# Kernel tuning notes

Measured on AMD Instinct MI355X. Metric: run time of the kernel, lower is better.

The kernel has to match this reference:

```python
import jax, jax.numpy as jnp
import numpy as np

C = 128       # in_channels
B = 256       # number of graph pairs (inter.shape[0])
N1_PER = 32   # nodes per graph, side 1
N2_PER = 32   # nodes per graph, side 2


def prelu(x, s):
    return jnp.where(x >= 0, x, s * x)


def _lin(k, fan_in, fan_out):
    return jax.random.normal(k, (fan_in, fan_out), jnp.float32) / np.sqrt(fan_in)


def setup_inputs() -> dict:
    key = jax.random.key(0)
    ks = jax.random.split(key, 16)
    N1, N2 = B * N1_PER, B * N2_PER
    d1 = np.full(B, N1_PER, np.int64)
    d2 = np.full(B, N2_PER, np.int64)
    batch_1 = np.repeat(np.arange(B), d1)
    batch_2 = np.repeat(np.arange(B), d2)
    # node offsets per graph (exclusive cumsum)
    s1 = np.concatenate([[0], np.cumsum(d1)[:-1]])
    s2 = np.concatenate([[0], np.cumsum(d2)[:-1]])
    # ragged pairwise cross-product indices, same as the torch loop
    ind_1 = np.concatenate([np.repeat(np.arange(d1[g]), d2[g]) + s1[g] for g in range(B)])
    ind_2 = np.concatenate([np.tile(np.arange(d2[g]), d1[g]) + s1[g] * 0 + s2[g] for g in range(B)])
    batch_ans = np.repeat(np.arange(B), d1 * d2)

    inp = {
        "x_1": jax.random.normal(ks[0], (N1, C), jnp.float32),
        "x_2": jax.random.normal(ks[1], (N2, C), jnp.float32),
        "inter": jax.random.normal(ks[2], (B, C), jnp.float32),
        "batch_1": jnp.asarray(batch_1, jnp.int32),
        "batch_2": jnp.asarray(batch_2, jnp.int32),
        "ind_1": jnp.asarray(ind_1, jnp.int32),
        "ind_2": jnp.asarray(ind_2, jnp.int32),
        "batch_ans": jnp.asarray(batch_ans, jnp.int32),
        # glorot-style param 'a'
        "a": jax.random.normal(ks[3], (C,), jnp.float32) * np.sqrt(2.0 / (1 + C)),
        # mlp: PReLU, Linear(2C,2C), PReLU, Linear(2C,C), PReLU, Linear(C,C)
        "Wm1": _lin(ks[4], 2 * C, 2 * C), "bm1": jnp.zeros((2 * C,), jnp.float32),
        "Wm2": _lin(ks[5], 2 * C, C),     "bm2": jnp.zeros((C,), jnp.float32),
        "Wm3": _lin(ks[6], C, C),         "bm3": jnp.zeros((C,), jnp.float32),
        "pm0": jnp.float32(0.25), "pm1": jnp.float32(0.25), "pm2": jnp.float32(0.25),
        # weight_1: Linear(2C,C), PReLU, Linear(C,1), Sigmoid
        "Wg1a": _lin(ks[7], 2 * C, C), "bg1a": jnp.zeros((C,), jnp.float32),
        "Wg1b": _lin(ks[8], C, 1),     "bg1b": jnp.zeros((1,), jnp.float32),
        "pw1": jnp.float32(0.25),
        # weight_2: Linear(2C,C), PReLU, Linear(C,1), Sigmoid
        "Wg2a": _lin(ks[9], 2 * C, C), "bg2a": jnp.zeros((C,), jnp.float32),
        "Wg2b": _lin(ks[10], C, 1),    "bg2b": jnp.zeros((1,), jnp.float32),
        "pw2": jnp.float32(0.25),
    }
    return inp


def reference(x_1, x_2, inter, batch_1, batch_2, ind_1, ind_2, batch_ans,
              a, Wm1, bm1, Wm2, bm2, Wm3, bm3, pm0, pm1, pm2,
              Wg1a, bg1a, Wg1b, bg1b, pw1, Wg2a, bg2a, Wg2b, bg2b, pw2):
    Bn = inter.shape[0]
    # global_add_pool readouts, broadcast back per node (repeat_interleave == gather by batch id)
    r1 = jax.ops.segment_sum(x_1, batch_1, num_segments=Bn)          # [B, C]
    r2 = jax.ops.segment_sum(x_2, batch_2, num_segments=Bn)          # [B, C]
    x1s = jnp.concatenate([x_1, r2[batch_1]], axis=1)                # [N1, 2C]
    x2s = jnp.concatenate([x_2, r1[batch_2]], axis=1)                # [N2, 2C]
    # gating MLPs -> sigmoid scalar per node
    w1 = jax.nn.sigmoid(prelu(x1s @ Wg1a + bg1a, pw1) @ Wg1b + bg1b)  # [N1, 1]
    w2 = jax.nn.sigmoid(prelu(x2s @ Wg2a + bg2a, pw2) @ Wg2b + bg2b)  # [N2, 1]
    x1g = x_1 * w1
    x2g = x_2 * w2
    # ragged pairwise gather
    xi = x1g[ind_1]                                                  # [P, C]
    xj = x2g[ind_2]                                                  # [P, C]
    h = jnp.concatenate([xi, xj], axis=1)                            # [P, 2C]
    h = prelu(h, pm0) @ Wm1 + bm1
    h = prelu(h, pm1) @ Wm2 + bm2
    h = prelu(h, pm2) @ Wm3 + bm3                                    # [P, C]
    ssi = (a * h) * inter[batch_ans]                                 # [P, C]
    logit = jax.ops.segment_sum(jnp.sum(ssi, axis=-1), batch_ans, num_segments=Bn)  # [B]
    return (logit, xi, xj)
```

## Files before the change

kernel.cpp:

```cpp
#include <hip/hip_runtime.h>
#include <hip/hip_bf16.h>
#include <hip/hip_fp16.h>

typedef __attribute__((ext_vector_type(8))) _Float16 half8;
typedef __attribute__((ext_vector_type(2))) _Float16 f16x2;
typedef __attribute__((ext_vector_type(8))) short short8;
typedef __attribute__((ext_vector_type(4))) float f32x4;

#define C_ 128

__device__ __forceinline__ unsigned short f2h(float f) {
    return __builtin_bit_cast(unsigned short, (_Float16)f);
}
__device__ __forceinline__ f16x2 pkrtz(float x, float y) {
    return __builtin_bit_cast(f16x2, __builtin_amdgcn_cvt_pkrtz(x, y));
}
__device__ __forceinline__ float prelu_f(float x, float s) {
    return fmaxf(x, 0.f) + s * fminf(x, 0.f);
}
__device__ __forceinline__ half8 prelu_h8(half8 x, half8 sl) {
    half8 z = {0, 0, 0, 0, 0, 0, 0, 0};
    half8 mx = __builtin_elementwise_max(x, z);
    half8 mn = __builtin_elementwise_min(x, z);
    return mn * sl + mx;
}

__global__ __launch_bounds__(256) void prep_weights(
    const float* __restrict__ Wm1, const float* __restrict__ Wm2,
    const float* __restrict__ Wg1a, const float* __restrict__ Wg2a,
    short* __restrict__ ws)
{
    int id = blockIdx.x * 256 + threadIdx.x;
    if (id < 8192) {
        int c = id >> 5, kb = (id & 31) * 8;
        short8 v;
        #pragma unroll
        for (int e = 0; e < 8; ++e) v[e] = (short)f2h(Wm1[(kb + e) * 256 + c]);
        *(short8*)(ws + c * 256 + kb) = v;
    }
    if (id < 4096) {
        int c = id >> 5, kb = (id & 31) * 8;
        short8 a, b, d;
        #pragma unroll
        for (int e = 0; e < 8; ++e) {
            a[e] = (short)f2h(Wm2 [(kb + e) * C_ + c]);
            b[e] = (short)f2h(Wg1a[(kb + e) * C_ + c]);
            d[e] = (short)f2h(Wg2a[(kb + e) * C_ + c]);
        }
        *(short8*)(ws + 65536  + c * 256 + kb) = a;
        *(short8*)(ws + 98304  + c * 256 + kb) = b;
        *(short8*)(ws + 131072 + c * 256 + kb) = d;
    }
}

__global__ __launch_bounds__(256) void reduce_out(
    const float* __restrict__ part, float* __restrict__ out)
{
    int t = threadIdx.x;
    out[t] = part[2 * t] + part[2 * t + 1];
}

__global__ __launch_bounds__(256, 2) void interactions_fused(
    const float* __restrict__ x1_, const float* __restrict__ x2_,
    const float* __restrict__ inter, const float* __restrict__ aP,
    const short* __restrict__ Wt,
    const float* __restrict__ bm1, const float* __restrict__ bm2,
    const float* __restrict__ Wm3, const float* __restrict__ bm3,
    const float* __restrict__ pm0p, const float* __restrict__ pm1p,
    const float* __restrict__ pm2p,
    const float* __restrict__ bg1a, const float* __restrict__ Wg1b,
    const float* __restrict__ bg1b, const float* __restrict__ pw1p,
    const float* __restrict__ bg2a, const float* __restrict__ Wg2b,
    const float* __restrict__ bg2b, const float* __restrict__ pw2p,
    float* __restrict__ part, float* __restrict__ out)
{
    __shared__ __align__(16) unsigned char regA[33792];
    __shared__ __align__(16) float rr[2][C_];
    __shared__ __align__(16) float tv[C_];
    __shared__ __align__(16) float ugs[C_];
    __shared__ float wgt[2][32];
    __shared__ float red[4];
    __shared__ float cbias_s;

    const int t = threadIdx.x;
    const int g = blockIdx.x >> 1;
    const int jh = blockIdx.x & 1;
    const int lane = t & 63;
    const int w = t >> 6;
    float* xs1 = (float*)regA;
    float* xs2 = (float*)(regA + 16896);

    {
        const float* s1 = x1_ + (size_t)g * 4096;
        const float* s2 = x2_ + (size_t)g * 4096;
        #pragma unroll
        for (int q = 0; q < 4; ++q) {
            int idx = q * 256 + t;
            int row = idx >> 5, cc = (idx & 31) * 4;
            float4 v1 = *(const float4*)(s1 + idx * 4);
            float4 v2 = *(const float4*)(s2 + idx * 4);
            *(float4*)(xs1 + row * 132 + cc) = v1;
            *(float4*)(xs2 + row * 132 + cc) = v2;
        }
    }
    __syncthreads();

    if (t < 128) {
        float s = 0.f;
        for (int n = 0; n < 32; ++n) s += xs1[n * 132 + t];
        rr[0][t] = s;
        tv[t] = aP[t] * inter[(size_t)g * C_ + t];
    } else {
        int c = t - 128;
        float s = 0.f;
        for (int n = 0; n < 32; ++n) s += xs2[n * 132 + c];
        rr[1][c] = s;
    }
    __syncthreads();

    if (t < 128) {
        const float* wr = Wm3 + t * C_;
        float s0 = 0, s1 = 0, s2 = 0, s3 = 0;
        #pragma unroll
        for (int k = 0; k < 128; k += 4) {
            float4 wv = *(const float4*)(wr + k);
            s0 += wv.x * tv[k];     s1 += wv.y * tv[k + 1];
            s2 += wv.z * tv[k + 2]; s3 += wv.w * tv[k + 3];
        }
        ugs[t] = (s0 + s1) + (s2 + s3);
    } else if (t < 192) {
        float p = bm3[lane] * tv[lane] + bm3[64 + lane] * tv[64 + lane];
        #pragma unroll
        for (int m = 1; m < 64; m <<= 1) p += __shfl_xor(p, m);
        if (lane == 0) cbias_s = p;
    }

    {
        const int sd = w >> 1;
        const int rt = w & 1;
        const float* xs = sd ? xs2 : xs1;
        const float* roth = sd ? rr[0] : rr[1];
        const short* WgT = Wt + (sd ? 131072 : 98304);
        const float* bga = sd ? bg2a : bg1a;
        const float* wgb = sd ? Wg2b : Wg1b;
        const float bgb = sd ? bg2b[0] : bg1b[0];
        const float pw  = sd ? pw2p[0] : pw1p[0];
        const int row = rt * 16 + (lane & 15);
        const int kg = (lane >> 4) * 8;

        half8 afr[8];
        #pragma unroll
        for (int kt = 0; kt < 8; ++kt) {
            const float* p = (kt < 4) ? (xs + row * 132 + kt * 32 + kg)
                                      : (roth + (kt - 4) * 32 + kg);
            float4 lo = *(const float4*)p;
            float4 hi = *(const float4*)(p + 4);
            f16x2 a = pkrtz(lo.x, lo.y);
            f16x2 b = pkrtz(lo.z, lo.w);
            f16x2 c = pkrtz(hi.x, hi.y);
            f16x2 d = pkrtz(hi.z, hi.w);
            half8 fr = {a[0], a[1], b[0], b[1], c[0], c[1], d[0], d[1]};
            afr[kt] = fr;
        }
        float pr[4] = {0, 0, 0, 0};
        #pragma unroll
        for (int ct = 0; ct < 8; ++ct) {
            const int c = ct * 16 + (lane & 15);
            const short* wp = WgT + c * 256 + kg;
            f32x4 acc = {0, 0, 0, 0};
            #pragma unroll
            for (int kt = 0; kt < 8; ++kt)
                acc = __builtin_amdgcn_mfma_f32_16x16x32_f16(
                          afr[kt], *(const half8*)(wp + kt * 32), acc, 0, 0, 0);
            const float bgac = bga[c], wgbc = wgb[c];
            #pragma unroll
            for (int r = 0; r < 4; ++r)
                pr[r] += prelu_f(acc[r] + bgac, pw) * wgbc;
        }
        #pragma unroll
        for (int r = 0; r < 4; ++r) {
            float p = pr[r];
            p += __shfl_xor(p, 1); p += __shfl_xor(p, 2);
            p += __shfl_xor(p, 4); p += __shfl_xor(p, 8);
            if ((lane & 15) == 0)
                wgt[sd][rt * 16 + (lane >> 4) * 4 + r] =
                    1.f / (1.f + __expf(-(p + bgb)));
        }
    }
    __syncthreads();

    float4 sl1[4], sl2[4];
    {
        const int cc = (t & 31) * 4;
        const int tn = t >> 5;
        #pragma unroll
        for (int m = 0; m < 4; ++m) {
            const int nr = m * 8 + tn;
            const float w1v = wgt[0][nr], w2v = wgt[1][nr];
            float4 v1 = *(float4*)(xs1 + nr * 132 + cc);
            float4 v2 = *(float4*)(xs2 + nr * 132 + cc);
            v1.x *= w1v; v1.y *= w1v; v1.z *= w1v; v1.w *= w1v;
            v2.x *= w2v; v2.y *= w2v; v2.z *= w2v; v2.w *= w2v;
            *(float4*)(xs1 + nr * 132 + cc) = v1;
            *(float4*)(xs2 + nr * 132 + cc) = v2;
            sl1[m] = v1; sl2[m] = v2;
        }
    }
    __syncthreads();

    {
        const int sd = w >> 1;
        const int rt = w & 1;
        const float* xs = sd ? xs2 : xs1;
        const float pm0 = pm0p[0];
        const int row = rt * 16 + (lane & 15);
        const int kg = (lane >> 4) * 8;
        half8 afr[4];
        #pragma unroll
        for (int kt = 0; kt < 4; ++kt) {
            const float* p = xs + row * 132 + kt * 32 + kg;
            float4 lo = *(const float4*)p;
            float4 hi = *(const float4*)(p + 4);
            f16x2 a = pkrtz(prelu_f(lo.x, pm0), prelu_f(lo.y, pm0));
            f16x2 b = pkrtz(prelu_f(lo.z, pm0), prelu_f(lo.w, pm0));
            f16x2 c = pkrtz(prelu_f(hi.x, pm0), prelu_f(hi.y, pm0));
            f16x2 d = pkrtz(prelu_f(hi.z, pm0), prelu_f(hi.w, pm0));
            half8 fr = {a[0], a[1], b[0], b[1], c[0], c[1], d[0], d[1]};
            afr[kt] = fr;
        }
        f32x4 acc[16];
        #pragma unroll
        for (int ct = 0; ct < 16; ++ct) {
            const int c = ct * 16 + (lane & 15);
            const short* wp = Wt + c * 256 + sd * 128 + kg;
            f32x4 av = {0, 0, 0, 0};
            #pragma unroll
            for (int kt = 0; kt < 4; ++kt)
                av = __builtin_amdgcn_mfma_f32_16x16x32_f16(
                         afr[kt], *(const half8*)(wp + kt * 32), av, 0, 0, 0);
            acc[ct] = av;
        }
        __syncthreads();
        unsigned char* dst = regA + (sd ? 16896 : 0);
        #pragma unroll
        for (int ct = 0; ct < 16; ++ct) {
            const int c = ct * 16 + (lane & 15);
            const float badd = sd ? 0.f : bm1[c];
            #pragma unroll
            for (int r = 0; r < 4; ++r) {
                const int n = rt * 16 + (lane >> 4) * 4 + r;
                const int off = n * 512 + ((2 * c + ((n & 7) << 6)) & 511);
                *(unsigned short*)(dst + off) = f2h(acc[ct][r] + badd);
            }
        }
    }
    __syncthreads();

    {
        const float pm1v = pm1p[0], pm2v = pm2p[0];
        const _Float16 pm1s = (_Float16)pm1v;
        const half8 pm1h = {pm1s, pm1s, pm1s, pm1s, pm1s, pm1s, pm1s, pm1s};
        const int cl = lane & 15;
        const int kg8 = (lane >> 4) * 8;
        const int kg16 = kg8 * 2;
        const int c0 = (2 * w) * 16 + cl, c1 = (2 * w + 1) * 16 + cl;
        half8 Bf0[8], Bf1[8];
        const short* w2p0 = Wt + 65536 + c0 * 256 + kg8;
        const short* w2p1 = Wt + 65536 + c1 * 256 + kg8;
        #pragma unroll
        for (int kt = 0; kt < 8; ++kt) {
            Bf0[kt] = *(const half8*)(w2p0 + kt * 32);
            Bf1[kt] = *(const half8*)(w2p1 + kt * 32);
        }
        const float bm2c0 = bm2[c0], bm2c1 = bm2[c1];
        const float ug0 = ugs[c0], ug1 = ugs[c1];
        const unsigned char* Ub = regA;
        const unsigned char* Vb = regA + 16896;

        half8 Vr[8];
        {
            const int j0 = jh * 16 + cl;
            const int vs = (j0 & 7) << 6;
            #pragma unroll
            for (int kt = 0; kt < 8; ++kt) {
                const int koff = kt * 64 + kg16;
                Vr[kt] = *(const half8*)(Vb + j0 * 512 + ((koff + vs) & 511));
            }
        }

        float* oxi = out + 256 + (size_t)g * 131072;
        float* oxj = out + 256 + 33554432 + (size_t)g * 131072;
        const int cc = (t & 31) * 4;
        const int tn = t >> 5;
        float psum = 0.f;

        #pragma unroll
        for (int rh = 0; rh < 2; ++rh) {
            const int n0 = rh * 16 + tn;
            const int n1 = rh * 16 + 8 + tn;
            const float4 s1a = sl1[rh * 2], s1b = sl1[rh * 2 + 1];
            const float4 s2a = sl2[rh * 2], s2b = sl2[rh * 2 + 1];
            #pragma unroll 2
            for (int ii = 0; ii < 16; ++ii) {
                const int i = rh * 16 + ii;
                const int ub = i * 512, us = (i & 7) << 6;
                half8 u8[8];
                #pragma unroll
                for (int kt = 0; kt < 8; ++kt)
                    u8[kt] = *(const half8*)(Ub + ub + ((kt * 64 + kg16 + us) & 511));
                f32x4 acc0 = {0, 0, 0, 0}, acc1 = {0, 0, 0, 0};
                #pragma unroll
                for (int kt = 0; kt < 8; ++kt) {
                    half8 af = prelu_h8(u8[kt] + Vr[kt], pm1h);
                    acc0 = __builtin_amdgcn_mfma_f32_16x16x32_f16(af, Bf0[kt], acc0, 0, 0, 0);
                    acc1 = __builtin_amdgcn_mfma_f32_16x16x32_f16(af, Bf1[kt], acc1, 0, 0, 0);
                }
                #pragma unroll
                for (int r = 0; r < 4; ++r) {
                    psum += prelu_f(acc0[r] + bm2c0, pm2v) * ug0;
                    psum += prelu_f(acc1[r] + bm2c1, pm2v) * ug1;
                }
                const int jj = jh * 16 + ii;
                *(float4*)(oxi + (size_t)(n0 * 32 + jj) * 128 + cc) = s1a;
                *(float4*)(oxi + (size_t)(n1 * 32 + jj) * 128 + cc) = s1b;
                *(float4*)(oxj + (size_t)(jj * 32 + n0) * 128 + cc) = s2a;
                *(float4*)(oxj + (size_t)(jj * 32 + n1) * 128 + cc) = s2b;
            }
        }
        #pragma unroll
        for (int m = 1; m < 64; m <<= 1) psum += __shfl_xor(psum, m);
        if (lane == 0) red[w] = psum;
    }
    __syncthreads();
    if (t == 0)
        part[blockIdx.x] = red[0] + red[1] + red[2] + red[3] + 512.f * cbias_s;
}

extern "C" void kernel_launch(void* const* d_in, const int* in_sizes, int n_in,
                              void* d_out, int out_size, void* d_ws, size_t ws_size,
                              hipStream_t stream) {
    const float* x1   = (const float*)d_in[0];
    const float* x2   = (const float*)d_in[1];
    const float* itr  = (const float*)d_in[2];
    const float* a    = (const float*)d_in[8];
    const float* Wm1  = (const float*)d_in[9];
    const float* bm1  = (const float*)d_in[10];
    const float* Wm2  = (const float*)d_in[11];
    const float* bm2  = (const float*)d_in[12];
    const float* Wm3  = (const float*)d_in[13];
    const float* bm3  = (const float*)d_in[14];
    const float* pm0  = (const float*)d_in[15];
    const float* pm1  = (const float*)d_in[16];
    const float* pm2  = (const float*)d_in[17];
    const float* Wg1a = (const float*)d_in[18];
    const float* bg1a = (const float*)d_in[19];
    const float* Wg1b = (const float*)d_in[20];
    const float* bg1b = (const float*)d_in[21];
    const float* pw1  = (const float*)d_in[22];
    const float* Wg2a = (const float*)d_in[23];
    const float* bg2a = (const float*)d_in[24];
    const float* Wg2b = (const float*)d_in[25];
    const float* bg2b = (const float*)d_in[26];
    const float* pw2  = (const float*)d_in[27];
    float* out = (float*)d_out;
    short* Wt = (short*)d_ws;
    float* part = (float*)(Wt + 163840);

    hipLaunchKernelGGL(prep_weights, dim3(32), dim3(256), 0, stream,
                       Wm1, Wm2, Wg1a, Wg2a, Wt);
    hipLaunchKernelGGL(interactions_fused, dim3(512), dim3(256), 0, stream,
                       x1, x2, itr, a, Wt, bm1, bm2, Wm3, bm3,
                       pm0, pm1, pm2, bg1a, Wg1b, bg1b, pw1,
                       bg2a, Wg2b, bg2b, pw2, part, out);
    hipLaunchKernelGGL(reduce_out, dim3(1), dim3(256), 0, stream,
                       part, out);
}
```

Baseline: 92.86 us.

## Warp-specialize one block per graph: MFMA waves compute while store waves write xi/xj

Each graph now runs as one 512-thread block instead of two 256-thread blocks. Four waves do the gating, the first layer and the pairwise MLP over all 32x32 pairs. The other four waves compute the Wm3 projection and stream the replicated xi/xj outputs with nontemporal stores, and the two groups coordinate through LDS atomic counters instead of full barriers. The final logit is written straight from the block, so the separate reduce kernel and its launch are gone. The intent is to overlap the large output writes with MFMA work and avoid duplicating the first layer across two blocks. The cost is lower occupancy (one block per CU) and spin-waiting on shared counters.

```diff
diff --git a/kernel.cpp b/kernel.cpp
--- a/kernel.cpp
+++ b/kernel.cpp
@@ -53,14 +53,7 @@
     }
 }
 
-__global__ __launch_bounds__(256) void reduce_out(
-    const float* __restrict__ part, float* __restrict__ out)
-{
-    int t = threadIdx.x;
-    out[t] = part[2 * t] + part[2 * t + 1];
-}
-
-__global__ __launch_bounds__(256, 2) void interactions_fused(
+__global__ __launch_bounds__(512, 1) void interactions_fused(
     const float* __restrict__ x1_, const float* __restrict__ x2_,
     const float* __restrict__ inter, const float* __restrict__ aP,
     const short* __restrict__ Wt,
@@ -72,35 +65,38 @@
     const float* __restrict__ bg1b, const float* __restrict__ pw1p,
     const float* __restrict__ bg2a, const float* __restrict__ Wg2b,
     const float* __restrict__ bg2b, const float* __restrict__ pw2p,
-    float* __restrict__ part, float* __restrict__ out)
+    float* __restrict__ out)
 {
-    __shared__ __align__(16) unsigned char regA[33792];
+    __shared__ __align__(16) float xs1[32 * 132];
+    __shared__ __align__(16) float xs2[32 * 132];
+    __shared__ __align__(16) unsigned char Ub[16384];
+    __shared__ __align__(16) unsigned char Vb[16384];
     __shared__ __align__(16) float rr[2][C_];
     __shared__ __align__(16) float tv[C_];
     __shared__ __align__(16) float ugs[C_];
-    __shared__ float wgt[2][32];
+    __shared__ float wgtp[2][2][32];
     __shared__ float red[4];
     __shared__ float cbias_s;
+    __shared__ int cnt1, cnt2;
 
     const int t = threadIdx.x;
-    const int g = blockIdx.x >> 1;
-    const int jh = blockIdx.x & 1;
+    const int g = blockIdx.x;
     const int lane = t & 63;
     const int w = t >> 6;
-    float* xs1 = (float*)regA;
-    float* xs2 = (float*)(regA + 16896);
+
+    if (t == 0) { cnt1 = 0; cnt2 = 0; }
 
     {
         const float* s1 = x1_ + (size_t)g * 4096;
         const float* s2 = x2_ + (size_t)g * 4096;
         #pragma unroll
-        for (int q = 0; q < 4; ++q) {
-            int idx = q * 256 + t;
+        for (int q = 0; q < 2; ++q) {
+            int idx = q * 512 + t;
             int row = idx >> 5, cc = (idx & 31) * 4;
-            float4 v1 = *(const float4*)(s1 + idx * 4);
-            float4 v2 = *(const float4*)(s2 + idx * 4);
-            *(float4*)(xs1 + row * 132 + cc) = v1;
-            *(float4*)(xs2 + row * 132 + cc) = v2;
+            f32x4 v1 = *(const f32x4*)(s1 + idx * 4);
+            f32x4 v2 = *(const f32x4*)(s2 + idx * 4);
+            *(f32x4*)(xs1 + row * 132 + cc) = v1;
+            *(f32x4*)(xs2 + row * 132 + cc) = v2;
         }
     }
     __syncthreads();
@@ -109,41 +105,27 @@
         float s = 0.f;
         for (int n = 0; n < 32; ++n) s += xs1[n * 132 + t];
         rr[0][t] = s;
-        tv[t] = aP[t] * inter[(size_t)g * C_ + t];
-    } else {
+    } else if (t < 256) {
         int c = t - 128;
         float s = 0.f;
         for (int n = 0; n < 32; ++n) s += xs2[n * 132 + c];
         rr[1][c] = s;
+    } else if (t < 384) {
+        int c = t - 256;
+        tv[c] = aP[c] * inter[(size_t)g * C_ + c];
     }
     __syncthreads();
 
-    if (t < 128) {
-        const float* wr = Wm3 + t * C_;
-        float s0 = 0, s1 = 0, s2 = 0, s3 = 0;
-        #pragma unroll
-        for (int k = 0; k < 128; k += 4) {
-            float4 wv = *(const float4*)(wr + k);
-            s0 += wv.x * tv[k];     s1 += wv.y * tv[k + 1];
-            s2 += wv.z * tv[k + 2]; s3 += wv.w * tv[k + 3];
-        }
-        ugs[t] = (s0 + s1) + (s2 + s3);
-    } else if (t < 192) {
-        float p = bm3[lane] * tv[lane] + bm3[64 + lane] * tv[64 + lane];
-        #pragma unroll
-        for (int m = 1; m < 64; m <<= 1) p += __shfl_xor(p, m);
-        if (lane == 0) cbias_s = p;
-    }
-
     {
-        const int sd = w >> 1;
-        const int rt = w & 1;
+        const int task = w & 3;
+        const int half = w >> 2;
+        const int sd = task >> 1;
+        const int rt = task & 1;
         const float* xs = sd ? xs2 : xs1;
         const float* roth = sd ? rr[0] : rr[1];
         const short* WgT = Wt + (sd ? 131072 : 98304);
         const float* bga = sd ? bg2a : bg1a;
         const float* wgb = sd ? Wg2b : Wg1b;
-        const float bgb = sd ? bg2b[0] : bg1b[0];
         const float pw  = sd ? pw2p[0] : pw1p[0];
         const int row = rt * 16 + (lane & 15);
         const int kg = (lane >> 4) * 8;
@@ -153,18 +135,19 @@
         for (int kt = 0; kt < 8; ++kt) {
             const float* p = (kt < 4) ? (xs + row * 132 + kt * 32 + kg)
                                       : (roth + (kt - 4) * 32 + kg);
-            float4 lo = *(const float4*)p;
-            float4 hi = *(const float4*)(p + 4);
-            f16x2 a = pkrtz(lo.x, lo.y);
-            f16x2 b = pkrtz(lo.z, lo.w);
-            f16x2 c = pkrtz(hi.x, hi.y);
-            f16x2 d = pkrtz(hi.z, hi.w);
+            f32x4 lo = *(const f32x4*)p;
+            f32x4 hi = *(const f32x4*)(p + 4);
+            f16x2 a = pkrtz(lo[0], lo[1]);
+            f16x2 b = pkrtz(lo[2], lo[3]);
+            f16x2 c = pkrtz(hi[0], hi[1]);
+            f16x2 d = pkrtz(hi[2], hi[3]);
             half8 fr = {a[0], a[1], b[0], b[1], c[0], c[1], d[0], d[1]};
             afr[kt] = fr;
         }
         float pr[4] = {0, 0, 0, 0};
         #pragma unroll
-        for (int ct = 0; ct < 8; ++ct) {
+        for (int cq = 0; cq < 4; ++cq) {
+            const int ct = half * 4 + cq;
             const int c = ct * 16 + (lane & 15);
             const short* wp = WgT + c * 256 + kg;
             f32x4 acc = {0, 0, 0, 0};
@@ -183,157 +166,197 @@
             p += __shfl_xor(p, 1); p += __shfl_xor(p, 2);
             p += __shfl_xor(p, 4); p += __shfl_xor(p, 8);
             if ((lane & 15) == 0)
-                wgt[sd][rt * 16 + (lane >> 4) * 4 + r] =
-                    1.f / (1.f + __expf(-(p + bgb)));
+                wgtp[half][sd][rt * 16 + (lane >> 4) * 4 + r] = p;
         }
     }
     __syncthreads();
 
-    float4 sl1[4], sl2[4];
     {
+        const float bgb1 = bg1b[0], bgb2 = bg2b[0];
         const int cc = (t & 31) * 4;
         const int tn = t >> 5;
         #pragma unroll
-        for (int m = 0; m < 4; ++m) {
-            const int nr = m * 8 + tn;
-            const float w1v = wgt[0][nr], w2v = wgt[1][nr];
-            float4 v1 = *(float4*)(xs1 + nr * 132 + cc);
-            float4 v2 = *(float4*)(xs2 + nr * 132 + cc);
-            v1.x *= w1v; v1.y *= w1v; v1.z *= w1v; v1.w *= w1v;
-            v2.x *= w2v; v2.y *= w2v; v2.z *= w2v; v2.w *= w2v;
-            *(float4*)(xs1 + nr * 132 + cc) = v1;
-            *(float4*)(xs2 + nr * 132 + cc) = v2;
-            sl1[m] = v1; sl2[m] = v2;
+        for (int m = 0; m < 2; ++m) {
+            const int nr = m * 16 + tn;
+            const float w1v = 1.f / (1.f + __expf(-(wgtp[0][0][nr] + wgtp[1][0][nr] + bgb1)));
+            const float w2v = 1.f / (1.f + __expf(-(wgtp[0][1][nr] + wgtp[1][1][nr] + bgb2)));
+            f32x4 v1 = *(f32x4*)(xs1 + nr * 132 + cc);
+            f32x4 v2 = *(f32x4*)(xs2 + nr * 132 + cc);
+            v1 *= w1v; v2 *= w2v;
+            *(f32x4*)(xs1 + nr * 132 + cc) = v1;
+            *(f32x4*)(xs2 + nr * 132 + cc) = v2;
         }
     }
     __syncthreads();
 
-    {
-        const int sd = w >> 1;
-        const int rt = w & 1;
-        const float* xs = sd ? xs2 : xs1;
-        const float pm0 = pm0p[0];
-        const int row = rt * 16 + (lane & 15);
-        const int kg = (lane >> 4) * 8;
-        half8 afr[4];
-        #pragma unroll
-        for (int kt = 0; kt < 4; ++kt) {
-            const float* p = xs + row * 132 + kt * 32 + kg;
-            float4 lo = *(const float4*)p;
-            float4 hi = *(const float4*)(p + 4);
-            f16x2 a = pkrtz(prelu_f(lo.x, pm0), prelu_f(lo.y, pm0));
-            f16x2 b = pkrtz(prelu_f(lo.z, pm0), prelu_f(lo.w, pm0));
-            f16x2 c = pkrtz(prelu_f(hi.x, pm0), prelu_f(hi.y, pm0));
-            f16x2 d = pkrtz(prelu_f(hi.z, pm0), prelu_f(hi.w, pm0));
-            half8 fr = {a[0], a[1], b[0], b[1], c[0], c[1], d[0], d[1]};
-            afr[kt] = fr;
-        }
-        f32x4 acc[16];
-        #pragma unroll
-        for (int ct = 0; ct < 16; ++ct) {
-            const int c = ct * 16 + (lane & 15);
-            const short* wp = Wt + c * 256 + sd * 128 + kg;
-            f32x4 av = {0, 0, 0, 0};
-            #pragma unroll
-            for (int kt = 0; kt < 4; ++kt)
-                av = __builtin_amdgcn_mfma_f32_16x16x32_f16(
-                         afr[kt], *(const half8*)(wp + kt * 32), av, 0, 0, 0);
-            acc[ct] = av;
-        }
-        __syncthreads();
-        unsigned char* dst = regA + (sd ? 16896 : 0);
-        #pragma unroll
-        for (int ct = 0; ct < 16; ++ct) {
-            const int c = ct * 16 + (lane & 15);
-            const float badd = sd ? 0.f : bm1[c];
-            #pragma unroll
-            for (int r = 0; r < 4; ++r) {
-                const int n = rt * 16 + (lane >> 4) * 4 + r;
-                const int off = n * 512 + ((2 * c + ((n & 7) << 6)) & 511);
-                *(unsigned short*)(dst + off) = f2h(acc[ct][r] + badd);
-            }
-        }
-    }
-    __syncthreads();
-
-    {
-        const float pm1v = pm1p[0], pm2v = pm2p[0];
-        const _Float16 pm1s = (_Float16)pm1v;
-        const half8 pm1h = {pm1s, pm1s, pm1s, pm1s, pm1s, pm1s, pm1s, pm1s};
-        const int cl = lane & 15;
-        const int kg8 = (lane >> 4) * 8;
-        const int kg16 = kg8 * 2;
-        const int c0 = (2 * w) * 16 + cl, c1 = (2 * w + 1) * 16 + cl;
-        half8 Bf0[8], Bf1[8];
-        const short* w2p0 = Wt + 65536 + c0 * 256 + kg8;
-        const short* w2p1 = Wt + 65536 + c1 * 256 + kg8;
-        #pragma unroll
-        for (int kt = 0; kt < 8; ++kt) {
-            Bf0[kt] = *(const half8*)(w2p0 + kt * 32);
-            Bf1[kt] = *(const half8*)(w2p1 + kt * 32);
-        }
-        const float bm2c0 = bm2[c0], bm2c1 = bm2[c1];
-        const float ug0 = ugs[c0], ug1 = ugs[c1];
-        const unsigned char* Ub = regA;
-        const unsigned char* Vb = regA + 16896;
-
-        half8 Vr[8];
-        {
-            const int j0 = jh * 16 + cl;
-            const int vs = (j0 & 7) << 6;
-            #pragma unroll
-            for (int kt = 0; kt < 8; ++kt) {
-                const int koff = kt * 64 + kg16;
-                Vr[kt] = *(const half8*)(Vb + j0 * 512 + ((koff + vs) & 511));
-            }
-        }
-
+    if (w >= 4) {
+        if (t < 384) {
+            const int c = t - 256;
+            const float* wr = Wm3 + c * C_;
+            float s0 = 0, s1 = 0, s2 = 0, s3 = 0;
+            #pragma unroll
+            for (int k = 0; k < 128; k += 4) {
+                f32x4 wv = *(const f32x4*)(wr + k);
+                s0 += wv[0] * tv[k];     s1 += wv[1] * tv[k + 1];
+                s2 += wv[2] * tv[k + 2]; s3 += wv[3] * tv[k + 3];
+            }
+            ugs[c] = (s0 + s1) + (s2 + s3);
+        } else if (w == 7) {
+            float p = bm3[lane] * tv[lane] + bm3[64 + lane] * tv[64 + lane];
+            #pragma unroll
+            for (int m = 1; m < 64; m <<= 1) p += __shfl_xor(p, m);
+            if (lane == 0) cbias_s = p;
+        }
+        __threadfence_block();
+        if (lane == 0)
+            __hip_atomic_fetch_add(&cnt1, 1, __ATOMIC_RELEASE, __HIP_MEMORY_SCOPE_WORKGROUP);
+
+        const int ws_ = w - 4;
         float* oxi = out + 256 + (size_t)g * 131072;
         float* oxj = out + 256 + 33554432 + (size_t)g * 131072;
-        const int cc = (t & 31) * 4;
-        const int tn = t >> 5;
+        const int ccl = (lane & 31) * 4;
+
+        #pragma unroll
+        for (int blk = 0; blk < 8; ++blk) {
+            const int i = ws_ * 8 + blk;
+            f32x4 v = *(const f32x4*)(xs1 + i * 132 + ccl);
+            float* base = oxi + i * 4096 + lane * 4;
+            #pragma unroll
+            for (int s2 = 0; s2 < 16; ++s2)
+                __builtin_nontemporal_store(v, (f32x4*)(base + s2 * 256));
+        }
+        f32x4 vj[16];
+        #pragma unroll
+        for (int s2 = 0; s2 < 16; ++s2) {
+            const int jn = (2 * s2 + (lane >> 5)) & 31;
+            vj[s2] = *(const f32x4*)(xs2 + jn * 132 + ccl);
+        }
+        #pragma unroll
+        for (int so = 0; so < 8; ++so) {
+            float* bb = oxj + (size_t)(ws_ * 256 + so * 32) * 128 + lane * 4;
+            #pragma unroll
+            for (int s2 = 0; s2 < 16; ++s2)
+                __builtin_nontemporal_store(vj[s2], (f32x4*)(bb + s2 * 256));
+        }
+    } else {
+        {
+            const int sd = w >> 1;
+            const int rt = w & 1;
+            const float* xs = sd ? xs2 : xs1;
+            const float pm0 = pm0p[0];
+            const int row = rt * 16 + (lane & 15);
+            const int kg = (lane >> 4) * 8;
+            half8 afr[4];
+            #pragma unroll
+            for (int kt = 0; kt < 4; ++kt) {
+                const float* p = xs + row * 132 + kt * 32 + kg;
+                f32x4 lo = *(const f32x4*)p;
+                f32x4 hi = *(const f32x4*)(p + 4);
+                f16x2 a = pkrtz(prelu_f(lo[0], pm0), prelu_f(lo[1], pm0));
+                f16x2 b = pkrtz(prelu_f(lo[2], pm0), prelu_f(lo[3], pm0));
+                f16x2 c = pkrtz(prelu_f(hi[0], pm0), prelu_f(hi[1], pm0));
+                f16x2 d = pkrtz(prelu_f(hi[2], pm0), prelu_f(hi[3], pm0));
+                half8 fr = {a[0], a[1], b[0], b[1], c[0], c[1], d[0], d[1]};
+                afr[kt] = fr;
+            }
+            unsigned char* dst = sd ? Vb : Ub;
+            #pragma unroll
+            for (int ct = 0; ct < 16; ++ct) {
+                const int c = ct * 16 + (lane & 15);
+                const short* wp = Wt + c * 256 + sd * 128 + kg;
+                f32x4 av = {0, 0, 0, 0};
+                #pragma unroll
+                for (int kt = 0; kt < 4; ++kt)
+                    av = __builtin_amdgcn_mfma_f32_16x16x32_f16(
+                             afr[kt], *(const half8*)(wp + kt * 32), av, 0, 0, 0);
+                const float badd = sd ? 0.f : bm1[c];
+                #pragma unroll
+                for (int r = 0; r < 4; ++r) {
+                    const int n = rt * 16 + (lane >> 4) * 4 + r;
+                    const int off = n * 512 + ((2 * c + ((n & 7) << 6)) & 511);
+                    *(unsigned short*)(dst + off) = f2h(av[r] + badd);
+                }
+            }
+        }
+        __threadfence_block();
+        if (lane == 0)
+            __hip_atomic_fetch_add(&cnt1, 1, __ATOMIC_RELEASE, __HIP_MEMORY_SCOPE_WORKGROUP);
+        while (__hip_atomic_load(&cnt1, __ATOMIC_ACQUIRE, __HIP_MEMORY_SCOPE_WORKGROUP) < 8)
+            __builtin_amdgcn_s_sleep(1);
+        __threadfence_block();
+
         float psum = 0.f;
-
-        #pragma unroll
-        for (int rh = 0; rh < 2; ++rh) {
-            const int n0 = rh * 16 + tn;
-            const int n1 = rh * 16 + 8 + tn;
-            const float4 s1a = sl1[rh * 2], s1b = sl1[rh * 2 + 1];
-            const float4 s2a = sl2[rh * 2], s2b = sl2[rh * 2 + 1];
+        {
+            const float pm1v = pm1p[0], pm2v = pm2p[0];
+            const _Float16 pm1s = (_Float16)pm1v;
+            const half8 pm1h = {pm1s, pm1s, pm1s, pm1s, pm1s, pm1s, pm1s, pm1s};
+            const int cl = lane & 15;
+            const int kg8 = (lane >> 4) * 8;
+            const int kg16 = kg8 * 2;
+            const int c0 = (2 * w) * 16 + cl, c1 = (2 * w + 1) * 16 + cl;
+            half8 Bf0[8], Bf1[8];
+            const short* w2p0 = Wt + 65536 + c0 * 256 + kg8;
+            const short* w2p1 = Wt + 65536 + c1 * 256 + kg8;
+            #pragma unroll
+            for (int kt = 0; kt < 8; ++kt) {
+                Bf0[kt] = *(const half8*)(w2p0 + kt * 32);
+                Bf1[kt] = *(const half8*)(w2p1 + kt * 32);
+            }
+            const float bm2c0 = bm2[c0], bm2c1 = bm2[c1];
+            const float ug0 = ugs[c0], ug1 = ugs[c1];
+
+            half8 VrA[8], VrB[8];
+            {
+                const int j0 = cl, j1 = 16 + cl;
+                #pragma unroll
+                for (int kt = 0; kt < 8; ++kt) {
+                    const int koff = kt * 64 + kg16;
+                    VrA[kt] = *(const half8*)(Vb + j0 * 512 + ((koff + ((j0 & 7) << 6)) & 511));
+                    VrB[kt] = *(const half8*)(Vb + j1 * 512 + ((koff + ((j1 & 7) << 6)) & 511));
+                }
+            }
+
             #pragma unroll 2
-            for (int ii = 0; ii < 16; ++ii) {
-                const int i = rh * 16 + ii;
+            for (int i = 0; i < 32; ++i) {
                 const int ub = i * 512, us = (i & 7) << 6;
                 half8 u8[8];
                 #pragma unroll
                 for (int kt = 0; kt < 8; ++kt)
                     u8[kt] = *(const half8*)(Ub + ub + ((kt * 64 + kg16 + us) & 511));
                 f32x4 acc0 = {0, 0, 0, 0}, acc1 = {0, 0, 0, 0};
+                f32x4 acc2 = {0, 0, 0, 0}, acc3 = {0, 0, 0, 0};
                 #pragma unroll
                 for (int kt = 0; kt < 8; ++kt) {
-                    half8 af = prelu_h8(u8[kt] + Vr[kt], pm1h);
-                    acc0 = __builtin_amdgcn_mfma_f32_16x16x32_f16(af, Bf0[kt], acc0, 0, 0, 0);
-                    acc1 = __builtin_amdgcn_mfma_f32_16x16x32_f16(af, Bf1[kt], acc1, 0, 0, 0);
+                    half8 afA = prelu_h8(u8[kt] + VrA[kt], pm1h);
+                    half8 afB = prelu_h8(u8[kt] + VrB[kt], pm1h);
+                    acc0 = __builtin_amdgcn_mfma_f32_16x16x32_f16(afA, Bf0[kt], acc0, 0, 0, 0);
+                    acc1 = __builtin_amdgcn_mfma_f32_16x16x32_f16(afA, Bf1[kt], acc1, 0, 0, 0);
+                    acc2 = __builtin_amdgcn_mfma_f32_16x16x32_f16(afB, Bf0[kt], acc2, 0, 0, 0);
+                    acc3 = __builtin_amdgcn_mfma_f32_16x16x32_f16(afB, Bf1[kt], acc3, 0, 0, 0);
                 }
                 #pragma unroll
                 for (int r = 0; r < 4; ++r) {
                     psum += prelu_f(acc0[r] + bm2c0, pm2v) * ug0;
                     psum += prelu_f(acc1[r] + bm2c1, pm2v) * ug1;
+                    psum += prelu_f(acc2[r] + bm2c0, pm2v) * ug0;
+                    psum += prelu_f(acc3[r] + bm2c1, pm2v) * ug1;
                 }
-                const int jj = jh * 16 + ii;
-                *(float4*)(oxi + (size_t)(n0 * 32 + jj) * 128 + cc) = s1a;
-                *(float4*)(oxi + (size_t)(n1 * 32 + jj) * 128 + cc) = s1b;
-                *(float4*)(oxj + (size_t)(jj * 32 + n0) * 128 + cc) = s2a;
-                *(float4*)(oxj + (size_t)(jj * 32 + n1) * 128 + cc) = s2b;
             }
         }
         #pragma unroll
         for (int m = 1; m < 64; m <<= 1) psum += __shfl_xor(psum, m);
-        if (lane == 0) red[w] = psum;
-    }
-    __syncthreads();
-    if (t == 0)
-        part[blockIdx.x] = red[0] + red[1] + red[2] + red[3] + 512.f * cbias_s;
+        if (lane == 0) {
+            red[w] = psum;
+            __threadfence_block();
+            __hip_atomic_fetch_add(&cnt2, 1, __ATOMIC_RELEASE, __HIP_MEMORY_SCOPE_WORKGROUP);
+            if (w == 0) {
+                while (__hip_atomic_load(&cnt2, __ATOMIC_ACQUIRE, __HIP_MEMORY_SCOPE_WORKGROUP) < 4)
+                    __builtin_amdgcn_s_sleep(1);
+                __threadfence_block();
+                out[g] = red[0] + red[1] + red[2] + red[3] + 1024.f * cbias_s;
+            }
+        }
+    }
 }
 
 extern "C" void kernel_launch(void* const* d_in, const int* in_sizes, int n_in,
@@ -364,14 +387,11 @@
     const float* pw2  = (const float*)d_in[27];
     float* out = (float*)d_out;
     short* Wt = (short*)d_ws;
-    float* part = (float*)(Wt + 163840);
 
     hipLaunchKernelGGL(prep_weights, dim3(32), dim3(256), 0, stream,
                        Wm1, Wm2, Wg1a, Wg2a, Wt);
-    hipLaunchKernelGGL(interactions_fused, dim3(512), dim3(256), 0, stream,
+    hipLaunchKernelGGL(interactions_fused, dim3(256), dim3(512), 0, stream,
                        x1, x2, itr, a, Wt, bm1, bm2, Wm3, bm3,
                        pm0, pm1, pm2, bg1a, Wg1b, bg1b, pw1,
-                       bg2a, Wg2b, bg2b, pw2, part, out);
-    hipLaunchKernelGGL(reduce_out, dim3(1), dim3(256), 0, stream,
-                       part, out);
-}
+                       bg2a, Wg2b, bg2b, pw2, out);
+}
```

New measurement: 86.34 us. -7.0%, faster.
